# Kernel optimization log

Hardware: AMD Instinct MI355X
Metric: run time of the kernel (lower is better)

## Reference

```python
import jax, jax.numpy as jnp
import numpy as np

DIM = 512   # model dim C (num_heads=1 -> head_dim = C)
NK = 128    # tokens per key-batch element
BQ = 512    # query batch
BK = 256    # key batch
NC = 1000   # num_classes for visual_fc head


def _ln(x, g, b, eps=1e-5):
    m = x.mean(-1, keepdims=True)
    v = x.var(-1, keepdims=True)
    return (x - m) * jax.lax.rsqrt(v + eps) * g + b


def _l2norm(x, eps=1e-12):  # F.normalize(p=2, dim=-1)
    n = jnp.linalg.norm(x, axis=-1, keepdims=True)
    return x / jnp.maximum(n, eps)


def setup_inputs() -> dict:
    key = jax.random.key(0)
    ks = jax.random.split(key, 8)
    s = 0.02
    return {
        "qx": jax.random.normal(ks[0], (BQ, 1, DIM), dtype=jnp.float32),
        "kx": jax.random.normal(ks[1], (BK, NK, DIM), dtype=jnp.float32),
        "key_padding_mask": jax.random.randint(ks[2], (BK, NK), 0, 2).astype(bool),
        "logit_scale": jnp.array([np.log(100.0)], dtype=jnp.float32),
        "g_q": jnp.ones((DIM,), jnp.float32), "b_q": jnp.zeros((DIM,), jnp.float32),
        "g_k": jnp.ones((DIM,), jnp.float32), "b_k": jnp.zeros((DIM,), jnp.float32),
        "wq": jax.random.normal(ks[3], (DIM, DIM), dtype=jnp.float32) * s,
        "wk": jax.random.normal(ks[4], (DIM, DIM), dtype=jnp.float32) * s,
        "w1": jax.random.normal(ks[5], (4 * DIM, DIM), dtype=jnp.float32) * s,
        "b1": jnp.zeros((4 * DIM,), jnp.float32),
        "w2": jax.random.normal(ks[6], (NC, 4 * DIM), dtype=jnp.float32) * s,
        "b2": jnp.zeros((NC,), jnp.float32),
    }


def reference(qx, kx, key_padding_mask, logit_scale,
              g_q, b_q, g_k, b_k, wq, wk, w1, b1, w2, b2):
    C = qx.shape[-1]
    scale = C ** -0.5  # num_heads=1 so head_dim == C
    # cross-batch single-query attention (Attention.forward)
    q = _ln(qx, g_q, b_q) @ wq.T                       # [Bq,1,C]
    k = _ln(kx, g_k, b_k) @ wk.T                       # [Bk,Nk,C]
    attn = jnp.einsum('qoc,knc->qkn', q, k) * scale    # [Bq,Bk,Nk]
    attn = jnp.where(key_padding_mask[None, :, :], -jnp.inf, attn)
    attn = jax.nn.softmax(attn, axis=-1)
    v = jnp.einsum('knc,qkn->qkc', kx, attn)           # [Bq,Bk,C]
    # two_branch head
    h = jax.nn.relu(qx[:, 0, :] @ w1.T + b1)           # [Bq,4C]
    x1 = h @ w2.T + b2                                 # [Bq,NC]
    x2 = jnp.einsum('qkc,qoc->qk', _l2norm(v), _l2norm(qx)) * jnp.exp(logit_scale)[0]
    return (x1, x2)
```

## Files before the change

### kernel.cpp

```cpp
#include <hip/hip_runtime.h>

typedef unsigned short u16;
typedef unsigned int u32;
typedef short bf16x8s __attribute__((ext_vector_type(8)));
typedef float f32x4 __attribute__((ext_vector_type(4)));

#define SCALE_C 0.044194173824159216f
#define MFMA16 __builtin_amdgcn_mfma_f32_16x16x32_bf16

__device__ __forceinline__ u16 f2bf(float f){
  union { float f; u32 u; } c; c.f = f;
  u32 u = c.u;
  return (u16)((u + 0x7fffu + ((u >> 16) & 1u)) >> 16);
}

__device__ __forceinline__ void gload16(const void* g, void* l){
  __builtin_amdgcn_global_load_lds((const __attribute__((address_space(1))) void*)g,
                                   (__attribute__((address_space(3))) void*)l, 16, 0, 0);
}

#define OFF_KXB  ((size_t)0)
#define OFF_G    (OFF_KXB + 33554432)
#define OFF_W2B  (OFF_G + 8388608)
#define OFF_H    (OFF_W2B + 4096000)
#define OFF_W1B  (OFF_H + 2097152)
#define OFF_QLN  (OFF_W1B + 2097152)
#define OFF_QHAT (OFF_QLN + 524288)
#define OFF_QXB  (OFF_QHAT + 524288)
#define OFF_P    (OFF_QXB + 524288)
#define OFF_M2   (OFF_P + 524288)
#define OFF_WQB  (OFF_M2 + 524288)
#define OFF_WCT  (OFF_WQB + 524288)
#define OFF_KM   (OFF_WCT + 524288)
#define OFF_KR   (OFF_KM + 131072)
#define OFF_T2   (OFF_KR + 131072)
#define OFF_FLAG (OFF_T2 + 4096)

__global__ __launch_bounds__(512) void k_phase0(
    const float* __restrict__ qx, const int* __restrict__ maskw,
    const float* __restrict__ g_q, const float* __restrict__ b_q,
    const float* __restrict__ wq, const float* __restrict__ wk,
    const float* __restrict__ b2,
    u16* __restrict__ qln, u16* __restrict__ qhat, u16* __restrict__ wct,
    float* __restrict__ t2s, int* __restrict__ flag, float* __restrict__ x1o)
{
  __shared__ __align__(16) u16 lBig[8192];
  __shared__ float redq[8][2];
  __shared__ int smax;
  const int bid = blockIdx.x, tid = threadIdx.x;
  const int lane = tid & 63, w = tid >> 6;
  const int l15 = lane & 15, lg = lane >> 4;

  if (bid < 256){
    const int row = bid*2 + (tid>>8);
    const int t = tid & 255;
    float2 v = *(const float2*)(qx + (size_t)row*512 + t*2);
    float s = v.x+v.y, sq = v.x*v.x+v.y*v.y;
    #pragma unroll
    for (int o = 1; o < 64; o <<= 1){ s += __shfl_xor(s,o); sq += __shfl_xor(sq,o); }
    if (lane == 0){ redq[w][0]=s; redq[w][1]=sq; }
    __syncthreads();
    const int h4 = (tid>>8)*4;
    s  = redq[h4][0]+redq[h4+1][0]+redq[h4+2][0]+redq[h4+3][0];
    sq = redq[h4][1]+redq[h4+1][1]+redq[h4+2][1]+redq[h4+3][1];
    float mean = s*(1.0f/512.0f);
    float var  = sq*(1.0f/512.0f) - mean*mean;
    float rstd = rsqrtf(var + 1e-5f);
    float il2  = 1.0f / fmaxf(sqrtf(sq), 1e-12f);
    float2 g  = *(const float2*)(g_q + t*2);
    float2 bb = *(const float2*)(b_q + t*2);
    u32 a  = f2bf((v.x-mean)*rstd*g.x+bb.x) | ((u32)f2bf((v.y-mean)*rstd*g.y+bb.y)<<16);
    u32 hh = f2bf(v.x*il2) | ((u32)f2bf(v.y*il2)<<16);
    *(u32*)(qln  + (size_t)row*512 + t*2) = a;
    *(u32*)(qhat + (size_t)row*512 + t*2) = hh;
  } else if (bid < 320){
    const int t = bid - 256;
    const int f0 = (t>>3)*64, c0 = (t&7)*64;
    const int w4 = w & 3;
    const int wr = (w4>>1)*32, wc = (w4&1)*32;
    u16* shA = lBig;
    u16* shB = lBig + 4096;
    f32x4 acc[2][2] = {};
    for (int i0 = 0; i0 < 512; i0 += 64){
      const int ii = tid >> 3;
      const int cc8 = (tid & 7) * 8;
      float4 va0 = *(const float4*)(wk + (size_t)(i0+ii)*512 + f0 + cc8);
      float4 va1 = *(const float4*)(wk + (size_t)(i0+ii)*512 + f0 + cc8 + 4);
      float4 vb0 = *(const float4*)(wq + (size_t)(i0+ii)*512 + c0 + cc8);
      float4 vb1 = *(const float4*)(wq + (size_t)(i0+ii)*512 + c0 + cc8 + 4);
      #pragma unroll
      for (int e = 0; e < 8; e++){
        float fa = e < 4 ? (&va0.x)[e] : (&va1.x)[e-4];
        float fb = e < 4 ? (&vb0.x)[e] : (&vb1.x)[e-4];
        int rowc = cc8 + e;
        int idx = rowc*64 + (((ii>>3) ^ (rowc&7))*8 + (ii&7));
        shA[idx] = f2bf(fa);
        shB[idx] = f2bf(fb);
      }
      __syncthreads();
      #pragma unroll
      for (int kk = 0; kk < 2; kk++){
        int cgr = kk*4 + lg;
        int ra0 = wr + l15, ra1 = wr + 16 + l15;
        int rb0 = wc + l15, rb1 = wc + 16 + l15;
        bf16x8s a0 = *(const bf16x8s*)&shA[ra0*64 + ((cgr ^ (ra0&7))*8)];
        bf16x8s a1 = *(const bf16x8s*)&shA[ra1*64 + ((cgr ^ (ra1&7))*8)];
        bf16x8s b0 = *(const bf16x8s*)&shB[rb0*64 + ((cgr ^ (rb0&7))*8)];
        bf16x8s b1 = *(const bf16x8s*)&shB[rb1*64 + ((cgr ^ (rb1&7))*8)];
        acc[0][0]=MFMA16(a0,b0,acc[0][0],0,0,0);
        acc[0][1]=MFMA16(a0,b1,acc[0][1],0,0,0);
        acc[1][0]=MFMA16(a1,b0,acc[1][0],0,0,0);
        acc[1][1]=MFMA16(a1,b1,acc[1][1],0,0,0);
      }
      __syncthreads();
    }
    if (tid < 256){
      #pragma unroll
      for (int i = 0; i < 2; i++)
        #pragma unroll
        for (int j = 0; j < 2; j++)
          #pragma unroll
          for (int r = 0; r < 4; r++)
            wct[(size_t)(f0 + wr + i*16 + lg*4 + r)*512 + c0 + wc + j*16 + l15]
                = f2bf(acc[i][j][r]);
    }
  } else if (bid < 570){
    int i = (bid-320)*2048 + tid*4;
    #pragma unroll
    for (int e = 0; e < 4; e++){
      int idx = i + e;
      x1o[idx] = b2[idx % 1000];
    }
  } else {
    if (tid == 0) smax = 0;
    t2s[tid] = 0.0f;
    __syncthreads();
    int mx = 0;
    for (int i = tid; i < 8192; i += 512){ int v = maskw[i]; mx = v > mx ? v : mx; }
    #pragma unroll
    for (int o = 1; o < 64; o <<= 1){ int t2 = __shfl_xor(mx,o); mx = t2 > mx ? t2 : mx; }
    if ((tid & 63) == 0) atomicMax(&smax, mx);
    __syncthreads();
    if (tid == 0) *flag = (smax <= 1) ? 1 : 0;
  }
}

__global__ __launch_bounds__(512) void k_phase1(
    const float* __restrict__ qx, const float* __restrict__ kx,
    const float* __restrict__ w1, const float* __restrict__ b1,
    const u16* __restrict__ qln, const u16* __restrict__ wct,
    const float* __restrict__ g_k,
    u16* __restrict__ kxb, float* __restrict__ km, float* __restrict__ kr,
    u16* __restrict__ Gm, u16* __restrict__ hbuf,
    u16* __restrict__ m2, float* __restrict__ t2s)
{
  __shared__ __align__(16) u16 lBig[16384];
  const int bid = blockIdx.x, tid = threadIdx.x;
  const int lane = tid & 63, w = tid >> 6;
  const int l15 = lane & 15, lg = lane >> 4;

  if (bid < 256){
    u16* lk = lBig;
    const int z = bid;
    const int a0 = (w>>2)*64, b0 = (w&3)*32;
    float s[16] = {0,0,0,0,0,0,0,0,0,0,0,0,0,0,0,0};
    float sq[16] = {0,0,0,0,0,0,0,0,0,0,0,0,0,0,0,0};
    f32x4 acc[4][2] = {};
    for (int ch = 0; ch < 4; ch++){
      #pragma unroll
      for (int i = 0; i < 16; i++){
        int r = w*16 + i;
        float2 v = *(const float2*)(kx + ((size_t)z*128 + r)*512 + ch*128 + lane*2);
        s[i] += v.x + v.y; sq[i] += v.x*v.x + v.y*v.y;
        u32 pk = f2bf(v.x) | ((u32)f2bf(v.y)<<16);
        *(u32*)(kxb + ((size_t)z*128 + r)*512 + ch*128 + lane*2) = pk;
        *(u32*)&lk[r*128 + ((lane*2) ^ ((r&7)<<3))] = pk;
      }
      __syncthreads();
      #pragma unroll
      for (int kk = 0; kk < 4; kk++){
        int cgr = kk*4 + lg;
        bf16x8s a[4], b[2];
        #pragma unroll
        for (int i2 = 0; i2 < 4; i2++){
          int r = a0 + i2*16 + l15;
          a[i2] = *(const bf16x8s*)&lk[r*128 + ((cgr*8) ^ ((r&7)<<3))];
        }
        #pragma unroll
        for (int j = 0; j < 2; j++){
          int r = b0 + j*16 + l15;
          b[j] = *(const bf16x8s*)&lk[r*128 + ((cgr*8) ^ ((r&7)<<3))];
        }
        #pragma unroll
        for (int i2 = 0; i2 < 4; i2++)
          #pragma unroll
          for (int j = 0; j < 2; j++)
            acc[i2][j] = MFMA16(a[i2], b[j], acc[i2][j], 0,0,0);
      }
      __syncthreads();
    }
    #pragma unroll
    for (int i = 0; i < 16; i++){
      float ss = s[i], qq = sq[i];
      #pragma unroll
      for (int o = 1; o < 64; o <<= 1){ ss += __shfl_xor(ss,o); qq += __shfl_xor(qq,o); }
      if (lane == 0){
        int r = w*16 + i;
        float mean = ss*(1.0f/512.0f);
        float var  = qq*(1.0f/512.0f) - mean*mean;
        km[z*128+r] = mean; kr[z*128+r] = rsqrtf(var + 1e-5f);
      }
    }
    u16* G = Gm + (size_t)z*16384;
    #pragma unroll
    for (int i2 = 0; i2 < 4; i2++)
      #pragma unroll
      for (int j = 0; j < 2; j++)
        #pragma unroll
        for (int r = 0; r < 4; r++)
          G[(size_t)(a0 + i2*16 + lg*4 + r)*128 + b0 + j*16 + l15] = f2bf(acc[i2][j][r]);
  } else if (bid < 384){
    const int t = bid - 256;
    const int m0 = (t >> 4)*64, n0 = (t & 15)*128;
    const int w4 = w & 3;
    const int nb = (w >> 2)*64;
    const int wr = (w4>>1)*32, wc = (w4&1)*32;
    u16* shA = lBig;
    u16* shB = lBig + 4096;
    f32x4 acc[2][2] = {};
    for (int kc = 0; kc < 512; kc += 64){
      {
        int row = tid >> 3, c8 = (tid & 7)*8;
        float4 a0 = *(const float4*)(qx + (size_t)(m0+row)*512 + kc + c8);
        float4 a1 = *(const float4*)(qx + (size_t)(m0+row)*512 + kc + c8 + 4);
        u16 ta[8] = {f2bf(a0.x),f2bf(a0.y),f2bf(a0.z),f2bf(a0.w),
                     f2bf(a1.x),f2bf(a1.y),f2bf(a1.z),f2bf(a1.w)};
        *(uint4*)&shA[row*64 + (((tid&7) ^ (row&7))*8)] = *(uint4*)ta;
        #pragma unroll
        for (int s2 = 0; s2 < 2; s2++){
          int u = tid + s2*512;
          int rowb = u >> 3, cb8 = (u & 7)*8;
          float4 b0 = *(const float4*)(w1 + (size_t)(n0+rowb)*512 + kc + cb8);
          float4 b1v = *(const float4*)(w1 + (size_t)(n0+rowb)*512 + kc + cb8 + 4);
          u16 tb[8] = {f2bf(b0.x),f2bf(b0.y),f2bf(b0.z),f2bf(b0.w),
                       f2bf(b1v.x),f2bf(b1v.y),f2bf(b1v.z),f2bf(b1v.w)};
          *(uint4*)&shB[rowb*64 + (((u&7) ^ (rowb&7))*8)] = *(uint4*)tb;
        }
      }
      __syncthreads();
      #pragma unroll
      for (int kk = 0; kk < 2; kk++){
        int cgr = kk*4 + lg;
        int ra0 = wr + l15, ra1 = wr + 16 + l15;
        int rb0 = nb + wc + l15, rb1 = nb + wc + 16 + l15;
        bf16x8s a0 = *(const bf16x8s*)&shA[ra0*64 + ((cgr ^ (ra0&7))*8)];
        bf16x8s a1 = *(const bf16x8s*)&shA[ra1*64 + ((cgr ^ (ra1&7))*8)];
        bf16x8s b0 = *(const bf16x8s*)&shB[rb0*64 + ((cgr ^ (rb0&7))*8)];
        bf16x8s b1 = *(const bf16x8s*)&shB[rb1*64 + ((cgr ^ (rb1&7))*8)];
        acc[0][0]=MFMA16(a0,b0,acc[0][0],0,0,0);
        acc[0][1]=MFMA16(a0,b1,acc[0][1],0,0,0);
        acc[1][0]=MFMA16(a1,b0,acc[1][0],0,0,0);
        acc[1][1]=MFMA16(a1,b1,acc[1][1],0,0,0);
      }
      __syncthreads();
    }
    #pragma unroll
    for (int i = 0; i < 2; i++)
      #pragma unroll
      for (int j = 0; j < 2; j++){
        int col = n0 + nb + wc + j*16 + l15;
        float bv = b1[col];
        #pragma unroll
        for (int r = 0; r < 4; r++){
          int row = m0 + wr + i*16 + lg*4 + r;
          hbuf[(size_t)row*2048 + col] = f2bf(fmaxf(acc[i][j][r] + bv, 0.0f));
        }
      }
  } else {
    const int b = bid - 384;
    const int m0 = (b>>3)*64, n0 = (b&7)*64;
    const int w4 = w & 3;
    const int wr = (w4>>1)*32, wc = (w4&1)*32;
    u16* shA = lBig;
    u16* shB = lBig + 4096;
    f32x4 acc[2][2] = {};
    for (int kc = 0; kc < 512; kc += 64){
      {
        int row = tid >> 3, cg = tid & 7;
        int sw = (cg ^ (row & 7)) * 8;
        *(uint4*)&shA[row*64 + sw] = *(const uint4*)(qln + (size_t)(m0+row)*512 + kc + cg*8);
        *(uint4*)&shB[row*64 + sw] = *(const uint4*)(wct + (size_t)(n0+row)*512 + kc + cg*8);
      }
      __syncthreads();
      #pragma unroll
      for (int kk = 0; kk < 2; kk++){
        int cgr = kk*4 + lg;
        int ra0 = wr + l15, ra1 = wr + 16 + l15;
        int rb0 = wc + l15, rb1 = wc + 16 + l15;
        bf16x8s a0 = *(const bf16x8s*)&shA[ra0*64 + ((cgr ^ (ra0&7))*8)];
        bf16x8s a1 = *(const bf16x8s*)&shA[ra1*64 + ((cgr ^ (ra1&7))*8)];
        bf16x8s b0 = *(const bf16x8s*)&shB[rb0*64 + ((cgr ^ (rb0&7))*8)];
        bf16x8s b1 = *(const bf16x8s*)&shB[rb1*64 + ((cgr ^ (rb1&7))*8)];
        acc[0][0]=MFMA16(a0,b0,acc[0][0],0,0,0);
        acc[0][1]=MFMA16(a0,b1,acc[0][1],0,0,0);
        acc[1][0]=MFMA16(a1,b0,acc[1][0],0,0,0);
        acc[1][1]=MFMA16(a1,b1,acc[1][1],0,0,0);
      }
      __syncthreads();
    }
    if (w < 4){
      #pragma unroll
      for (int i = 0; i < 2; i++){
        #pragma unroll
        for (int r = 0; r < 4; r++){
          int row = m0 + wr + i*16 + lg*4 + r;
          float part = 0.f;
          #pragma unroll
          for (int j = 0; j < 2; j++){
            int col = n0 + wc + j*16 + l15;
            float e = SCALE_C * acc[i][j][r] * g_k[col];
            m2[(size_t)row*512 + col] = f2bf(e);
            part += e;
          }
          #pragma unroll
          for (int o = 1; o < 16; o <<= 1) part += __shfl_xor(part, o);
          if (l15 == 0) atomicAdd(&t2s[row], part);
        }
      }
    }
  }
}

__global__ __launch_bounds__(512, 4) void k_attn(
    const u16* __restrict__ kxb, const u16* __restrict__ Gm,
    const u16* __restrict__ m2, const u16* __restrict__ qhat,
    const float* __restrict__ km, const float* __restrict__ kr,
    const float* __restrict__ t2s, const void* __restrict__ maskp,
    const int* __restrict__ flagp, const float* __restrict__ lsp,
    float* __restrict__ x2,
    const u16* __restrict__ hbuf, const float* __restrict__ w2,
    float* __restrict__ x1o)
{
  __shared__ __align__(16) u16 sb[24576];
  __shared__ float lt2[128];
  __shared__ float lNum[128][2], lDen[128][2];
  u16* lP = sb;

  const int tid = threadIdx.x, lane = tid & 63, w = tid >> 6;
  const int l15 = lane & 15, lg = lane >> 4;

  if (blockIdx.x < 64){
    const int t = blockIdx.x*4 + blockIdx.y;
    const int tile = t >> 2, ks = t & 3;
    const int m0 = (tile>>3)*64, n0 = (tile&7)*128;
    const int wr = (w >> 2)*32, wc = (w & 3)*32;
    u16* lA = sb;
    u16* lB = sb + 4096;
    f32x4 acc[2][2] = {};
    for (int kc = ks*512; kc < ks*512 + 512; kc += 64){
      {
        int row = tid >> 3, cg = tid & 7;
        *(uint4*)&lA[row*64 + ((cg ^ (row&7))*8)] =
            *(const uint4*)(hbuf + (size_t)(m0+row)*2048 + kc + cg*8);
        #pragma unroll
        for (int s2 = 0; s2 < 2; s2++){
          int u = tid + s2*512;
          int rowb = u >> 3, cb8 = (u & 7)*8;
          uint4 vb = make_uint4(0,0,0,0);
          if (n0 + rowb < 1000){
            float4 b0 = *(const float4*)(w2 + (size_t)(n0+rowb)*2048 + kc + cb8);
            float4 b1v = *(const float4*)(w2 + (size_t)(n0+rowb)*2048 + kc + cb8 + 4);
            u16 tb[8] = {f2bf(b0.x),f2bf(b0.y),f2bf(b0.z),f2bf(b0.w),
                         f2bf(b1v.x),f2bf(b1v.y),f2bf(b1v.z),f2bf(b1v.w)};
            vb = *(uint4*)tb;
          }
          *(uint4*)&lB[rowb*64 + (((u&7) ^ (rowb&7))*8)] = vb;
        }
      }
      __syncthreads();
      #pragma unroll
      for (int kk = 0; kk < 2; kk++){
        int cgr = kk*4 + lg;
        int ra0 = wr + l15, ra1 = wr + 16 + l15;
        int rb0 = wc + l15, rb1 = wc + 16 + l15;
        bf16x8s a0 = *(const bf16x8s*)&lA[ra0*64 + ((cgr ^ (ra0&7))*8)];
        bf16x8s a1 = *(const bf16x8s*)&lA[ra1*64 + ((cgr ^ (ra1&7))*8)];
        bf16x8s b0 = *(const bf16x8s*)&lB[rb0*64 + ((cgr ^ (rb0&7))*8)];
        bf16x8s b1 = *(const bf16x8s*)&lB[rb1*64 + ((cgr ^ (rb1&7))*8)];
        acc[0][0]=MFMA16(a0,b0,acc[0][0],0,0,0);
        acc[0][1]=MFMA16(a0,b1,acc[0][1],0,0,0);
        acc[1][0]=MFMA16(a1,b0,acc[1][0],0,0,0);
        acc[1][1]=MFMA16(a1,b1,acc[1][1],0,0,0);
      }
      __syncthreads();
    }
    #pragma unroll
    for (int i = 0; i < 2; i++)
      #pragma unroll
      for (int j = 0; j < 2; j++){
        int col = n0 + wc + j*16 + l15;
        if (col < 1000){
          #pragma unroll
          for (int r = 0; r < 4; r++){
            int row = m0 + wr + i*16 + lg*4 + r;
            atomicAdd(&x1o[(size_t)row*1000 + col], acc[i][j][r]);
          }
        }
      }
    return;
  }

  const int kb = blockIdx.x - 64, q0 = blockIdx.y * 128;
  const int wr = (w >> 1)*32, wcol = (w & 1)*64;
  const int fl = *flagp;
  const float expls = __expf(lsp[0]);

  if (tid < 128) lt2[tid] = t2s[q0 + tid];

  float kmv[4], krv[4], mbv[4];
  #pragma unroll
  for (int j = 0; j < 4; j++){
    int gn = kb*128 + wcol + j*16 + l15;
    kmv[j] = km[gn]; krv[j] = kr[gn];
    int mv = fl ? ((const int*)maskp)[gn] : (int)((const unsigned char*)maskp)[gn];
    mbv[j] = mv ? -1e30f : 0.0f;
  }

  const u16* KX = kxb + (size_t)kb * 65536;
  f32x4 aS[2][4] = {}, aD[2][4] = {};

  const int srow  = w*16 + (lane >> 2);
  const int sslot = (lane & 3) ^ ((srow >> 1) & 3);
  const int lofs  = w*512;

  #define STAGE(p) do{                                                         \
    const int kc_ = (p)*32;                                                    \
    u16* b_ = sb + ((p)&1)*12288;                                              \
    gload16(KX   + (size_t)srow*512      + kc_ + sslot*8, b_ + lofs);          \
    gload16(m2   + (size_t)(q0+srow)*512 + kc_ + sslot*8, b_ + 4096 + lofs);   \
    gload16(qhat + (size_t)(q0+srow)*512 + kc_ + sslot*8, b_ + 8192 + lofs);   \
  }while(0)

  STAGE(0);
  #pragma unroll
  for (int p = 0; p < 16; p++){
    if (p < 15){
      STAGE(p+1);
      asm volatile("s_waitcnt vmcnt(3)" ::: "memory");
    } else {
      asm volatile("s_waitcnt vmcnt(0)" ::: "memory");
    }
    __builtin_amdgcn_s_barrier();
    __builtin_amdgcn_sched_barrier(0);
    const u16* lb  = sb + (p&1)*12288;
    const u16* lKX = lb;
    const u16* lM2 = lb + 4096;
    const u16* lQH = lb + 8192;
    const int rA0 = wr + l15, rA1 = wr + 16 + l15;
    bf16x8s am0 = *(const bf16x8s*)&lM2[rA0*32 + ((lg ^ ((rA0>>1)&3))*8)];
    bf16x8s am1 = *(const bf16x8s*)&lM2[rA1*32 + ((lg ^ ((rA1>>1)&3))*8)];
    bf16x8s aq0 = *(const bf16x8s*)&lQH[rA0*32 + ((lg ^ ((rA0>>1)&3))*8)];
    bf16x8s aq1 = *(const bf16x8s*)&lQH[rA1*32 + ((lg ^ ((rA1>>1)&3))*8)];
    __builtin_amdgcn_s_setprio(1);
    #pragma unroll
    for (int j = 0; j < 4; j++){
      int rB = wcol + j*16 + l15;
      bf16x8s bk = *(const bf16x8s*)&lKX[rB*32 + ((lg ^ ((rB>>1)&3))*8)];
      aS[0][j] = MFMA16(am0, bk, aS[0][j], 0,0,0);
      aS[1][j] = MFMA16(am1, bk, aS[1][j], 0,0,0);
      aD[0][j] = MFMA16(aq0, bk, aD[0][j], 0,0,0);
      aD[1][j] = MFMA16(aq1, bk, aD[1][j], 0,0,0);
    }
    __builtin_amdgcn_s_setprio(0);
    __builtin_amdgcn_sched_barrier(0);
    __builtin_amdgcn_s_barrier();
  }
  __syncthreads();

  #pragma unroll
  for (int i = 0; i < 2; i++){
    #pragma unroll
    for (int r = 0; r < 4; r++){
      int rowl = wr + i*16 + lg*4 + r;
      float t2v = lt2[rowl];
      float sn = 0.f;
      #pragma unroll
      for (int j = 0; j < 4; j++){
        float L = krv[j]*(aS[i][j][r] - kmv[j]*t2v) + mbv[j];
        float e = __expf(L);
        aS[i][j][r] = e;
        sn += e * aD[i][j][r];
      }
      #pragma unroll
      for (int o = 1; o < 16; o <<= 1) sn += __shfl_xor(sn, o);
      if (l15 == 0) lNum[rowl][w&1] = sn;
      #pragma unroll
      for (int j = 0; j < 4; j++){
        int n = wcol + j*16 + l15;
        lP[rowl*128 + ((n>>3)^(rowl&7))*8 + (n&7)] = f2bf(aS[i][j][r]);
      }
    }
  }
  __syncthreads();

  f32x4 aT[2][4] = {};
  const u16* Gk = Gm + (size_t)kb * 16384;
  #pragma unroll
  for (int kk = 0; kk < 4; kk++){
    int cgr = kk*4 + lg;
    int rA0 = wr + l15, rA1 = wr + 16 + l15;
    bf16x8s p0 = *(const bf16x8s*)&lP[rA0*128 + ((cgr^(rA0&7))*8)];
    bf16x8s p1 = *(const bf16x8s*)&lP[rA1*128 + ((cgr^(rA1&7))*8)];
    #pragma unroll
    for (int j = 0; j < 4; j++){
      int mcol = wcol + j*16 + l15;
      bf16x8s bg = *(const bf16x8s*)(Gk + (size_t)mcol*128 + kk*32 + lg*8);
      aT[0][j] = MFMA16(p0, bg, aT[0][j], 0,0,0);
      aT[1][j] = MFMA16(p1, bg, aT[1][j], 0,0,0);
    }
  }
  #pragma unroll
  for (int i = 0; i < 2; i++){
    #pragma unroll
    for (int r = 0; r < 4; r++){
      int rowl = wr + i*16 + lg*4 + r;
      float sd = 0.f;
      #pragma unroll
      for (int j = 0; j < 4; j++) sd += aT[i][j][r] * aS[i][j][r];
      #pragma unroll
      for (int o = 1; o < 16; o <<= 1) sd += __shfl_xor(sd, o);
      if (l15 == 0) lDen[rowl][w&1] = sd;
    }
  }
  __syncthreads();

  if (tid < 128){
    float num  = lNum[tid][0] + lNum[tid][1];
    float den2 = lDen[tid][0] + lDen[tid][1];
    float den  = fmaxf(sqrtf(fmaxf(den2, 0.0f)), 1e-12f);
    x2[(size_t)(q0 + tid)*256 + kb] = expls * num / den;
  }
}

extern "C" void kernel_launch(void* const* d_in, const int* in_sizes, int n_in,
                              void* d_out, int out_size, void* d_ws, size_t ws_size,
                              hipStream_t stream)
{
  (void)in_sizes; (void)n_in; (void)out_size; (void)ws_size;
  const float* qx  = (const float*)d_in[0];
  const float* kx  = (const float*)d_in[1];
  const void*  mask= d_in[2];
  const float* lsp = (const float*)d_in[3];
  const float* g_q = (const float*)d_in[4];
  const float* b_q = (const float*)d_in[5];
  const float* g_k = (const float*)d_in[6];
  const float* wq  = (const float*)d_in[8];
  const float* wk  = (const float*)d_in[9];
  const float* w1  = (const float*)d_in[10];
  const float* b1  = (const float*)d_in[11];
  const float* w2  = (const float*)d_in[12];
  const float* b2  = (const float*)d_in[13];

  char* ws = (char*)d_ws;
  u16* kxb  = (u16*)(ws + OFF_KXB);
  u16* Gm   = (u16*)(ws + OFF_G);
  u16* hbuf = (u16*)(ws + OFF_H);
  u16* qln  = (u16*)(ws + OFF_QLN);
  u16* qhat = (u16*)(ws + OFF_QHAT);
  u16* m2   = (u16*)(ws + OFF_M2);
  u16* wct  = (u16*)(ws + OFF_WCT);
  float* km  = (float*)(ws + OFF_KM);
  float* kr  = (float*)(ws + OFF_KR);
  float* t2s = (float*)(ws + OFF_T2);
  int*   flag= (int*)(ws + OFF_FLAG);
  float* x1o = (float*)d_out;
  float* x2o = (float*)d_out + 512*1000;

  k_phase0<<<dim3(571), dim3(512), 0, stream>>>(
      qx, (const int*)mask, g_q, b_q, wq, wk, b2,
      qln, qhat, wct, t2s, flag, x1o);
  k_phase1<<<dim3(448), dim3(512), 0, stream>>>(
      qx, kx, w1, b1, qln, wct, g_k,
      kxb, km, kr, Gm, hbuf, m2, t2s);
  k_attn<<<dim3(320, 4), dim3(512), 0, stream>>>(
      kxb, Gm, m2, qhat, km, kr, t2s, mask, flag, lsp, x2o,
      hbuf, w2, x1o);
}
```

Before: 126.5 us.

## Split x1 GEMM into own kernel and process two key batches per attention block

Moves the x1 = h·w2ᵀ GEMM out of the fused attention kernel into a separate 64x64-tiled kernel launched beforehand. The attention kernel now uses 1024-thread blocks that each handle two key-batch elements, so the staged m2/qhat query tiles are loaded once and reused across both key batches, halving their global traffic. The cost is an extra kernel launch, serialization of the x1 GEMM before attention instead of running them concurrently, and larger blocks with more LDS that may reduce occupancy.

```diff
diff --git a/kernel.cpp b/kernel.cpp
--- a/kernel.cpp
+++ b/kernel.cpp
@@ -331,87 +331,86 @@
   }
 }
 
-__global__ __launch_bounds__(512, 4) void k_attn(
+__global__ __launch_bounds__(256) void k_x1(
+    const u16* __restrict__ hbuf, const float* __restrict__ w2,
+    float* __restrict__ x1o)
+{
+  __shared__ __align__(16) u16 lA[64][64], lB[64][64];
+  const int b = blockIdx.x;
+  const int ks = b >> 7;
+  const int t  = b & 127;
+  const int m0 = (t >> 4)*64, n0 = (t & 15)*64;
+  const int tid = threadIdx.x, lane = tid & 63, w = tid >> 6;
+  const int wr = (w>>1)*32, wc = (w&1)*32;
+  const int l15 = lane & 15, lg = lane >> 4;
+  f32x4 acc[2][2] = {};
+  for (int kc = ks*512; kc < ks*512 + 512; kc += 64){
+    #pragma unroll
+    for (int s = 0; s < 2; s++){
+      int u = tid + s*256;
+      int row = u >> 3, cg = u & 7;
+      int sw = (cg ^ (row & 7)) * 8;
+      *(uint4*)&lA[row][sw] = *(const uint4*)(hbuf + (size_t)(m0+row)*2048 + kc + cg*8);
+      uint4 vb = make_uint4(0,0,0,0);
+      if (n0 + row < 1000){
+        float4 b0 = *(const float4*)(w2 + (size_t)(n0+row)*2048 + kc + cg*8);
+        float4 b1v = *(const float4*)(w2 + (size_t)(n0+row)*2048 + kc + cg*8 + 4);
+        u16 tb[8] = {f2bf(b0.x),f2bf(b0.y),f2bf(b0.z),f2bf(b0.w),
+                     f2bf(b1v.x),f2bf(b1v.y),f2bf(b1v.z),f2bf(b1v.w)};
+        vb = *(uint4*)tb;
+      }
+      *(uint4*)&lB[row][sw] = vb;
+    }
+    __syncthreads();
+    #pragma unroll
+    for (int kk = 0; kk < 2; kk++){
+      int cgr = kk*4 + lg;
+      int ra0 = wr + l15, ra1 = wr + 16 + l15;
+      int rb0 = wc + l15, rb1 = wc + 16 + l15;
+      bf16x8s a0 = *(const bf16x8s*)&lA[ra0][(cgr ^ (ra0&7))*8];
+      bf16x8s a1 = *(const bf16x8s*)&lA[ra1][(cgr ^ (ra1&7))*8];
+      bf16x8s b0 = *(const bf16x8s*)&lB[rb0][(cgr ^ (rb0&7))*8];
+      bf16x8s b1 = *(const bf16x8s*)&lB[rb1][(cgr ^ (rb1&7))*8];
+      acc[0][0]=MFMA16(a0,b0,acc[0][0],0,0,0);
+      acc[0][1]=MFMA16(a0,b1,acc[0][1],0,0,0);
+      acc[1][0]=MFMA16(a1,b0,acc[1][0],0,0,0);
+      acc[1][1]=MFMA16(a1,b1,acc[1][1],0,0,0);
+    }
+    __syncthreads();
+  }
+  #pragma unroll
+  for (int i = 0; i < 2; i++)
+    #pragma unroll
+    for (int j = 0; j < 2; j++){
+      int col = n0 + wc + j*16 + l15;
+      if (col < 1000){
+        #pragma unroll
+        for (int r = 0; r < 4; r++){
+          int row = m0 + wr + i*16 + lg*4 + r;
+          atomicAdd(&x1o[(size_t)row*1000 + col], acc[i][j][r]);
+        }
+      }
+    }
+}
+
+__global__ __launch_bounds__(1024, 4) void k_attn(
     const u16* __restrict__ kxb, const u16* __restrict__ Gm,
     const u16* __restrict__ m2, const u16* __restrict__ qhat,
     const float* __restrict__ km, const float* __restrict__ kr,
     const float* __restrict__ t2s, const void* __restrict__ maskp,
     const int* __restrict__ flagp, const float* __restrict__ lsp,
-    float* __restrict__ x2,
-    const u16* __restrict__ hbuf, const float* __restrict__ w2,
-    float* __restrict__ x1o)
+    float* __restrict__ x2)
 {
-  __shared__ __align__(16) u16 sb[24576];
+  __shared__ __align__(16) u16 sb[32768];
   __shared__ float lt2[128];
-  __shared__ float lNum[128][2], lDen[128][2];
+  __shared__ float lNum[128][4], lDen[128][4];
   u16* lP = sb;
 
+  const int kp = blockIdx.x, q0 = blockIdx.y * 128;
   const int tid = threadIdx.x, lane = tid & 63, w = tid >> 6;
+  const int rg = w & 3, cg = w >> 2;
+  const int wr = rg*32, wcol = cg*64;
   const int l15 = lane & 15, lg = lane >> 4;
-
-  if (blockIdx.x < 64){
-    const int t = blockIdx.x*4 + blockIdx.y;
-    const int tile = t >> 2, ks = t & 3;
-    const int m0 = (tile>>3)*64, n0 = (tile&7)*128;
-    const int wr = (w >> 2)*32, wc = (w & 3)*32;
-    u16* lA = sb;
-    u16* lB = sb + 4096;
-    f32x4 acc[2][2] = {};
-    for (int kc = ks*512; kc < ks*512 + 512; kc += 64){
-      {
-        int row = tid >> 3, cg = tid & 7;
-        *(uint4*)&lA[row*64 + ((cg ^ (row&7))*8)] =
-            *(const uint4*)(hbuf + (size_t)(m0+row)*2048 + kc + cg*8);
-        #pragma unroll
-        for (int s2 = 0; s2 < 2; s2++){
-          int u = tid + s2*512;
-          int rowb = u >> 3, cb8 = (u & 7)*8;
-          uint4 vb = make_uint4(0,0,0,0);
-          if (n0 + rowb < 1000){
-            float4 b0 = *(const float4*)(w2 + (size_t)(n0+rowb)*2048 + kc + cb8);
-            float4 b1v = *(const float4*)(w2 + (size_t)(n0+rowb)*2048 + kc + cb8 + 4);
-            u16 tb[8] = {f2bf(b0.x),f2bf(b0.y),f2bf(b0.z),f2bf(b0.w),
-                         f2bf(b1v.x),f2bf(b1v.y),f2bf(b1v.z),f2bf(b1v.w)};
-            vb = *(uint4*)tb;
-          }
-          *(uint4*)&lB[rowb*64 + (((u&7) ^ (rowb&7))*8)] = vb;
-        }
-      }
-      __syncthreads();
-      #pragma unroll
-      for (int kk = 0; kk < 2; kk++){
-        int cgr = kk*4 + lg;
-        int ra0 = wr + l15, ra1 = wr + 16 + l15;
-        int rb0 = wc + l15, rb1 = wc + 16 + l15;
-        bf16x8s a0 = *(const bf16x8s*)&lA[ra0*64 + ((cgr ^ (ra0&7))*8)];
-        bf16x8s a1 = *(const bf16x8s*)&lA[ra1*64 + ((cgr ^ (ra1&7))*8)];
-        bf16x8s b0 = *(const bf16x8s*)&lB[rb0*64 + ((cgr ^ (rb0&7))*8)];
-        bf16x8s b1 = *(const bf16x8s*)&lB[rb1*64 + ((cgr ^ (rb1&7))*8)];
-        acc[0][0]=MFMA16(a0,b0,acc[0][0],0,0,0);
-        acc[0][1]=MFMA16(a0,b1,acc[0][1],0,0,0);
-        acc[1][0]=MFMA16(a1,b0,acc[1][0],0,0,0);
-        acc[1][1]=MFMA16(a1,b1,acc[1][1],0,0,0);
-      }
-      __syncthreads();
-    }
-    #pragma unroll
-    for (int i = 0; i < 2; i++)
-      #pragma unroll
-      for (int j = 0; j < 2; j++){
-        int col = n0 + wc + j*16 + l15;
-        if (col < 1000){
-          #pragma unroll
-          for (int r = 0; r < 4; r++){
-            int row = m0 + wr + i*16 + lg*4 + r;
-            atomicAdd(&x1o[(size_t)row*1000 + col], acc[i][j][r]);
-          }
-        }
-      }
-    return;
-  }
-
-  const int kb = blockIdx.x - 64, q0 = blockIdx.y * 128;
-  const int wr = (w >> 1)*32, wcol = (w & 1)*64;
   const int fl = *flagp;
   const float expls = __expf(lsp[0]);
 
@@ -420,25 +419,27 @@
   float kmv[4], krv[4], mbv[4];
   #pragma unroll
   for (int j = 0; j < 4; j++){
-    int gn = kb*128 + wcol + j*16 + l15;
+    int gn = kp*256 + wcol + j*16 + l15;
     kmv[j] = km[gn]; krv[j] = kr[gn];
     int mv = fl ? ((const int*)maskp)[gn] : (int)((const unsigned char*)maskp)[gn];
     mbv[j] = mv ? -1e30f : 0.0f;
   }
 
-  const u16* KX = kxb + (size_t)kb * 65536;
+  const u16* KXp = kxb + (size_t)kp * 131072;
   f32x4 aS[2][4] = {}, aD[2][4] = {};
 
-  const int srow  = w*16 + (lane >> 2);
-  const int sslot = (lane & 3) ^ ((srow >> 1) & 3);
-  const int lofs  = w*512;
-
-  #define STAGE(p) do{                                                         \
-    const int kc_ = (p)*32;                                                    \
-    u16* b_ = sb + ((p)&1)*12288;                                              \
-    gload16(KX   + (size_t)srow*512      + kc_ + sslot*8, b_ + lofs);          \
-    gload16(m2   + (size_t)(q0+srow)*512 + kc_ + sslot*8, b_ + 4096 + lofs);   \
-    gload16(qhat + (size_t)(q0+srow)*512 + kc_ + sslot*8, b_ + 8192 + lofs);   \
+  const int srowK  = w*16 + (lane >> 2);
+  const int sslotK = (lane & 3) ^ ((srowK >> 1) & 3);
+  const int srowQ  = (w & 7)*16 + (lane >> 2);
+  const int sslotQ = (lane & 3) ^ ((srowQ >> 1) & 3);
+  const u16* QS   = (w < 8) ? m2 : qhat;
+  const int  ldst = (w < 8) ? (8192 + w*512) : (12288 + (w-8)*512);
+
+  #define STAGE(p) do{                                                        \
+    const int kc_ = (p)*32;                                                   \
+    u16* b_ = sb + ((p)&1)*16384;                                             \
+    gload16(KXp + (size_t)srowK*512      + kc_ + sslotK*8, b_ + w*512);       \
+    gload16(QS  + (size_t)(q0+srowQ)*512 + kc_ + sslotQ*8, b_ + ldst);        \
   }while(0)
 
   STAGE(0);
@@ -446,16 +447,16 @@
   for (int p = 0; p < 16; p++){
     if (p < 15){
       STAGE(p+1);
-      asm volatile("s_waitcnt vmcnt(3)" ::: "memory");
+      asm volatile("s_waitcnt vmcnt(2)" ::: "memory");
     } else {
       asm volatile("s_waitcnt vmcnt(0)" ::: "memory");
     }
     __builtin_amdgcn_s_barrier();
     __builtin_amdgcn_sched_barrier(0);
-    const u16* lb  = sb + (p&1)*12288;
+    const u16* lb  = sb + (p&1)*16384;
     const u16* lKX = lb;
-    const u16* lM2 = lb + 4096;
-    const u16* lQH = lb + 8192;
+    const u16* lM2 = lb + 8192;
+    const u16* lQH = lb + 12288;
     const int rA0 = wr + l15, rA1 = wr + 16 + l15;
     bf16x8s am0 = *(const bf16x8s*)&lM2[rA0*32 + ((lg ^ ((rA0>>1)&3))*8)];
     bf16x8s am1 = *(const bf16x8s*)&lM2[rA1*32 + ((lg ^ ((rA1>>1)&3))*8)];
@@ -493,27 +494,29 @@
       }
       #pragma unroll
       for (int o = 1; o < 16; o <<= 1) sn += __shfl_xor(sn, o);
-      if (l15 == 0) lNum[rowl][w&1] = sn;
+      if (l15 == 0) lNum[rowl][cg] = sn;
       #pragma unroll
       for (int j = 0; j < 4; j++){
         int n = wcol + j*16 + l15;
-        lP[rowl*128 + ((n>>3)^(rowl&7))*8 + (n&7)] = f2bf(aS[i][j][r]);
+        lP[rowl*256 + (((n>>3) ^ (rowl&7))*8) + (n&7)] = f2bf(aS[i][j][r]);
       }
     }
   }
   __syncthreads();
 
   f32x4 aT[2][4] = {};
-  const u16* Gk = Gm + (size_t)kb * 16384;
+  const int h = cg >> 1;
+  const u16* Gk = Gm + (size_t)(kp*2 + h) * 16384;
+  const int c64 = (cg & 1) * 64;
   #pragma unroll
   for (int kk = 0; kk < 4; kk++){
-    int cgr = kk*4 + lg;
+    int slot = h*16 + kk*4 + lg;
     int rA0 = wr + l15, rA1 = wr + 16 + l15;
-    bf16x8s p0 = *(const bf16x8s*)&lP[rA0*128 + ((cgr^(rA0&7))*8)];
-    bf16x8s p1 = *(const bf16x8s*)&lP[rA1*128 + ((cgr^(rA1&7))*8)];
+    bf16x8s p0 = *(const bf16x8s*)&lP[rA0*256 + ((slot ^ (rA0&7))*8)];
+    bf16x8s p1 = *(const bf16x8s*)&lP[rA1*256 + ((slot ^ (rA1&7))*8)];
     #pragma unroll
     for (int j = 0; j < 4; j++){
-      int mcol = wcol + j*16 + l15;
+      int mcol = c64 + j*16 + l15;
       bf16x8s bg = *(const bf16x8s*)(Gk + (size_t)mcol*128 + kk*32 + lg*8);
       aT[0][j] = MFMA16(p0, bg, aT[0][j], 0,0,0);
       aT[1][j] = MFMA16(p1, bg, aT[1][j], 0,0,0);
@@ -529,16 +532,17 @@
       for (int j = 0; j < 4; j++) sd += aT[i][j][r] * aS[i][j][r];
       #pragma unroll
       for (int o = 1; o < 16; o <<= 1) sd += __shfl_xor(sd, o);
-      if (l15 == 0) lDen[rowl][w&1] = sd;
+      if (l15 == 0) lDen[rowl][cg] = sd;
     }
   }
   __syncthreads();
 
-  if (tid < 128){
-    float num  = lNum[tid][0] + lNum[tid][1];
-    float den2 = lDen[tid][0] + lDen[tid][1];
+  if (tid < 256){
+    int rowl = tid & 127, h2 = tid >> 7;
+    float num  = lNum[rowl][h2*2] + lNum[rowl][h2*2+1];
+    float den2 = lDen[rowl][h2*2] + lDen[rowl][h2*2+1];
     float den  = fmaxf(sqrtf(fmaxf(den2, 0.0f)), 1e-12f);
-    x2[(size_t)(q0 + tid)*256 + kb] = expls * num / den;
+    x2[(size_t)(q0 + rowl)*256 + kp*2 + h2] = expls * num / den;
   }
 }
 
@@ -582,7 +586,7 @@
   k_phase1<<<dim3(448), dim3(512), 0, stream>>>(
       qx, kx, w1, b1, qln, wct, g_k,
       kxb, km, kr, Gm, hbuf, m2, t2s);
-  k_attn<<<dim3(320, 4), dim3(512), 0, stream>>>(
-      kxb, Gm, m2, qhat, km, kr, t2s, mask, flag, lsp, x2o,
-      hbuf, w2, x1o);
-}
+  k_x1<<<dim3(512), dim3(256), 0, stream>>>(hbuf, w2, x1o);
+  k_attn<<<dim3(128, 4), dim3(1024), 0, stream>>>(
+      kxb, Gm, m2, qhat, km, kr, t2s, mask, flag, lsp, x2o);
+}
```

Measured after the change: 134.5 us. 1.06x slower.
